# Optimization experiments

Measured on AMD Instinct MI355X. Metric: run time of the kernel, lower is better.

## Reference

```python
import jax, jax.numpy as jnp
import numpy as np

D_MODEL = 1024


def setup_inputs() -> dict:
    key = jax.random.key(0)
    ks = jax.random.split(key, 8)
    B, S, D = 2, 2048, D_MODEL
    s = 1.0 / np.sqrt(D)
    causal = jnp.where(jnp.tril(jnp.ones((S, S), dtype=bool)), 0.0, -1e9)[None, None]
    return {
        "query": jax.random.normal(ks[0], (B, S, D), jnp.float32),
        "key": jax.random.normal(ks[1], (B, S, D), jnp.float32),
        "value": jax.random.normal(ks[2], (B, S, D), jnp.float32),
        "padding_mask": jnp.zeros((B, 1, 1, S), jnp.float32),
        "lookahead_mask": causal.astype(jnp.float32),
        "w_q": jax.random.normal(ks[3], (D, D), jnp.float32) * s,
        "w_k": jax.random.normal(ks[4], (D, D), jnp.float32) * s,
        "w_v": jax.random.normal(ks[5], (D, D), jnp.float32) * s,
        "w_out": jax.random.normal(ks[6], (D, D), jnp.float32) * s,
        "b_q": jnp.zeros((D,), jnp.float32),
        "b_k": jnp.zeros((D,), jnp.float32),
        "b_v": jnp.zeros((D,), jnp.float32),
        "b_out": jnp.zeros((D,), jnp.float32),
        "n_heads": 16,
    }


def reference(query, key, value, padding_mask, lookahead_mask,
              w_q, w_k, w_v, w_out, b_q, b_k, b_v, b_out, n_heads):
    B, S, D = query.shape
    d_k = D // n_heads
    # projections (torch Linear: x @ W.T + b; here weights stored as (in, out))
    q = (query @ w_q + b_q).reshape(B, S, n_heads, d_k).transpose(0, 2, 1, 3)
    k = (key @ w_k + b_k).reshape(B, S, n_heads, d_k).transpose(0, 2, 1, 3)
    v = (value @ w_v + b_v).reshape(B, S, n_heads, d_k).transpose(0, 2, 1, 3)
    scores = jnp.einsum("bhqd,bhkd->bhqk", q, k) / jnp.sqrt(jnp.float32(d_k))
    scores = scores + padding_mask + lookahead_mask
    attn = jax.nn.softmax(scores, axis=-1)
    out = jnp.einsum("bhqk,bhkd->bhqd", attn, v)
    out = out.transpose(0, 2, 1, 3).reshape(B, S, D)
    return out @ w_out + b_out
```

## Files before the change

### kernel.cpp

```cpp
#include <hip/hip_runtime.h>
#include <hip/hip_bf16.h>
#include <stdint.h>

typedef __bf16 bf16x8 __attribute__((ext_vector_type(8)));
typedef __bf16 bf16x4 __attribute__((ext_vector_type(4)));
typedef float f32x4 __attribute__((ext_vector_type(4)));

#define DMODEL 1024
#define SEQ    2048
#define NHEAD  16
#define DK     64
#define MTOT   4096
#define KDIM   1024

#define DRAIN_VM_LGKM() asm volatile("s_waitcnt vmcnt(0) lgkmcnt(0)" ::: "memory")
#define DRAIN_LGKM()    asm volatile("s_waitcnt lgkmcnt(0)" ::: "memory")

__device__ __forceinline__ void gl2lds16(const void* g, void* l) {
  __builtin_amdgcn_global_load_lds((__attribute__((address_space(1))) void*)(g),
                                   (__attribute__((address_space(3))) void*)(l),
                                   16, 0, 0);
}

__global__ __launch_bounds__(256) void k_cvt3(const float* __restrict__ q,
                                              const float* __restrict__ k,
                                              const float* __restrict__ v,
                                              __bf16* __restrict__ oq,
                                              __bf16* __restrict__ ok,
                                              __bf16* __restrict__ ov,
                                              int n4) {
  const int which = blockIdx.y;
  const float* in = which == 0 ? q : (which == 1 ? k : v);
  __bf16* out = which == 0 ? oq : (which == 1 ? ok : ov);
  const int i = blockIdx.x * 256 + threadIdx.x;
  if (i >= n4) return;
  const float4 f = ((const float4*)in)[i];
  bf16x4 o = { (__bf16)f.x, (__bf16)f.y, (__bf16)f.z, (__bf16)f.w };
  ((bf16x4*)out)[i] = o;
}

__global__ __launch_bounds__(256) void k_transpose4(const float* __restrict__ w0,
                                                    const float* __restrict__ w1,
                                                    const float* __restrict__ w2,
                                                    const float* __restrict__ w3,
                                                    __bf16* __restrict__ t0,
                                                    __bf16* __restrict__ t1,
                                                    __bf16* __restrict__ t2,
                                                    __bf16* __restrict__ t3) {
  const int z = blockIdx.z;
  const float* W = z == 0 ? w0 : (z == 1 ? w1 : (z == 2 ? w2 : w3));
  __bf16* WT = z == 0 ? t0 : (z == 1 ? t1 : (z == 2 ? t2 : t3));
  __shared__ float tile[32][33];
  int n0 = blockIdx.x * 32, k0 = blockIdx.y * 32;
  int tx = threadIdx.x & 31, ty = threadIdx.x >> 5;
  #pragma unroll
  for (int i = ty; i < 32; i += 8)
    tile[i][tx] = W[(size_t)(k0 + i) * DMODEL + n0 + tx];
  __syncthreads();
  #pragma unroll
  for (int i = ty; i < 32; i += 8)
    WT[(size_t)(n0 + i) * DMODEL + k0 + tx] = (__bf16)tile[tx][i];
}

__global__ __launch_bounds__(256) void k_gemm_qkv(
    const __bf16* __restrict__ A0, const __bf16* __restrict__ A1, const __bf16* __restrict__ A2,
    const __bf16* __restrict__ W0, const __bf16* __restrict__ W1, const __bf16* __restrict__ W2,
    const float* __restrict__ bi0, const float* __restrict__ bi1, const float* __restrict__ bi2,
    __bf16* __restrict__ C0, __bf16* __restrict__ C1, __bf16* __restrict__ C2) {
  const int z = blockIdx.z;
  const __bf16* A  = z == 0 ? A0 : (z == 1 ? A1 : A2);
  const __bf16* BT = z == 0 ? W0 : (z == 1 ? W1 : W2);
  const float* bias = z == 0 ? bi0 : (z == 1 ? bi1 : bi2);
  __bf16* Cout = z == 0 ? C0 : (z == 1 ? C1 : C2);

  __shared__ __align__(16) __bf16 As[128 * 32];
  __shared__ __align__(16) __bf16 Bs[128 * 32];
  const int tid = threadIdx.x;
  const int lane = tid & 63;
  const int wv = tid >> 6;
  const int wm = wv >> 1, wn = wv & 1;
  const int m0 = blockIdx.y * 128, n0 = blockIdx.x * 128;
  const int lr = lane & 15, lg = lane >> 4;

  f32x4 acc[4][4] = {};

  for (int k0 = 0; k0 < KDIM; k0 += 32) {
    #pragma unroll
    for (int i = 0; i < 2; ++i) {
      int c = tid + i * 256;
      int row = c >> 2, seg = c & 3;
      gl2lds16(A + (size_t)(m0 + row) * KDIM + k0 + seg * 8, (char*)As + c * 16);
      gl2lds16(BT + (size_t)(n0 + row) * KDIM + k0 + seg * 8, (char*)Bs + c * 16);
    }
    DRAIN_VM_LGKM();
    __syncthreads();
    bf16x8 af[4], bfr[4];
    #pragma unroll
    for (int mi = 0; mi < 4; ++mi)
      af[mi] = *(const bf16x8*)&As[(wm * 64 + mi * 16 + lr) * 32 + lg * 8];
    #pragma unroll
    for (int ni = 0; ni < 4; ++ni)
      bfr[ni] = *(const bf16x8*)&Bs[(wn * 64 + ni * 16 + lr) * 32 + lg * 8];
    #pragma unroll
    for (int mi = 0; mi < 4; ++mi)
      #pragma unroll
      for (int ni = 0; ni < 4; ++ni)
        acc[mi][ni] = __builtin_amdgcn_mfma_f32_16x16x32_bf16(af[mi], bfr[ni], acc[mi][ni], 0, 0, 0);
    DRAIN_LGKM();
    __syncthreads();
  }

  #pragma unroll
  for (int mi = 0; mi < 4; ++mi)
    #pragma unroll
    for (int ni = 0; ni < 4; ++ni) {
      const int col = n0 + wn * 64 + ni * 16 + lr;
      const float bv = bias[col];
      #pragma unroll
      for (int r = 0; r < 4; ++r) {
        const int row = m0 + wm * 64 + mi * 16 + lg * 4 + r;
        float v = acc[mi][ni][r] + bv;
        const int b = row >> 11, s = row & (SEQ - 1);
        const int h = col >> 6, dd = col & (DK - 1);
        if (z == 2)
          Cout[((size_t)(b * NHEAD + h) * DK + dd) * SEQ + s] = (__bf16)v;
        else
          Cout[((size_t)(b * NHEAD + h) * SEQ + s) * DK + dd] = (__bf16)v;
      }
    }
}

__global__ __launch_bounds__(256) void k_gemm_out(const __bf16* __restrict__ A,
                                                  const __bf16* __restrict__ BT,
                                                  const float* __restrict__ bias,
                                                  float* __restrict__ Cout) {
  __shared__ __align__(16) __bf16 As[128 * 32];
  __shared__ __align__(16) __bf16 Bs[128 * 32];
  const int tid = threadIdx.x;
  const int lane = tid & 63;
  const int wv = tid >> 6;
  const int wm = wv >> 1, wn = wv & 1;
  const int m0 = blockIdx.y * 128, n0 = blockIdx.x * 128;
  const int lr = lane & 15, lg = lane >> 4;

  f32x4 acc[4][4] = {};

  for (int k0 = 0; k0 < KDIM; k0 += 32) {
    #pragma unroll
    for (int i = 0; i < 2; ++i) {
      int c = tid + i * 256;
      int row = c >> 2, seg = c & 3;
      gl2lds16(A + (size_t)(m0 + row) * KDIM + k0 + seg * 8, (char*)As + c * 16);
      gl2lds16(BT + (size_t)(n0 + row) * KDIM + k0 + seg * 8, (char*)Bs + c * 16);
    }
    DRAIN_VM_LGKM();
    __syncthreads();
    bf16x8 af[4], bfr[4];
    #pragma unroll
    for (int mi = 0; mi < 4; ++mi)
      af[mi] = *(const bf16x8*)&As[(wm * 64 + mi * 16 + lr) * 32 + lg * 8];
    #pragma unroll
    for (int ni = 0; ni < 4; ++ni)
      bfr[ni] = *(const bf16x8*)&Bs[(wn * 64 + ni * 16 + lr) * 32 + lg * 8];
    #pragma unroll
    for (int mi = 0; mi < 4; ++mi)
      #pragma unroll
      for (int ni = 0; ni < 4; ++ni)
        acc[mi][ni] = __builtin_amdgcn_mfma_f32_16x16x32_bf16(af[mi], bfr[ni], acc[mi][ni], 0, 0, 0);
    DRAIN_LGKM();
    __syncthreads();
  }

  #pragma unroll
  for (int mi = 0; mi < 4; ++mi)
    #pragma unroll
    for (int ni = 0; ni < 4; ++ni) {
      const int col = n0 + wn * 64 + ni * 16 + lr;
      const float bv = bias[col];
      #pragma unroll
      for (int r = 0; r < 4; ++r) {
        const int row = m0 + wm * 64 + mi * 16 + lg * 4 + r;
        Cout[(size_t)row * DMODEL + col] = acc[mi][ni][r] + bv;
      }
    }
}

__global__ __launch_bounds__(256, 4) void k_attn(const __bf16* __restrict__ Q,
                                                 const __bf16* __restrict__ Kt,
                                                 const __bf16* __restrict__ Vt,
                                                 const float* __restrict__ pmask,
                                                 float* __restrict__ Op0,
                                                 float* __restrict__ Op1,
                                                 float* __restrict__ ML) {
  __shared__ __align__(16) __bf16 Ks[2][64 * 64];
  __shared__ __align__(16) __bf16 Vs[2][64 * 64];
  __shared__ __align__(16) __bf16 plds[4][16 * 64];

  const int tid = threadIdx.x;
  const int lane = tid & 63, wv = tid >> 6;
  const int lr = lane & 15, lg = lane >> 4;

  const int bid = blockIdx.x;
  const int xcd = bid & 7;
  const int rdec = bid >> 3;
  const int slot = rdec >> 5;
  const int rem = rdec & 31;
  const int pair = rem >> 1;
  const int s = rem & 1;
  const int bh = slot * 8 + xcd;
  const int b = bh >> 4, h = bh & 15;

  const __bf16* Qb = Q + (size_t)bh * SEQ * DK;
  const __bf16* Kb = Kt + (size_t)bh * SEQ * DK;
  const __bf16* Vb = Vt + (size_t)bh * DK * SEQ;
  const float* pm = pmask + (size_t)b * SEQ;
  float* Op = s ? Op1 : Op0;
  const float SCL = 0.125f * 1.44269504f;
  const float L2E = 1.44269504f;

  auto stage = [&](int buf, int t) {
    #pragma unroll
    for (int i = 0; i < 2; ++i) {
      const int c = tid + i * 256;
      const int row = c >> 3;
      const int sx = ((c & 7) * 16) ^ ((row & 7) << 4);
      gl2lds16((const char*)Kb + (size_t)(t * 64 + row) * 128 + sx,
               (char*)&Ks[buf][0] + c * 16);
      gl2lds16((const char*)Vb + (size_t)row * (SEQ * 2) + (size_t)t * 128 + sx,
               (char*)&Vs[buf][0] + c * 16);
    }
  };

  for (int half = 0; half < 2; ++half) {
    const int qb = half ? (31 - pair) : pair;
    const int nt = qb + 1;
    const int QR = qb * 64 + wv * 16;

    const bf16x8 qf0 = *(const bf16x8*)&Qb[(size_t)(QR + lr) * DK + lg * 8];
    const bf16x8 qf1 = *(const bf16x8*)&Qb[(size_t)(QR + lr) * DK + 32 + lg * 8];

    float mrow = -1e30f, lrw = 0.f;
    f32x4 oacc[4] = {};

    int t = s;
    if (t < nt) {
      stage(0, t);
      DRAIN_VM_LGKM();
      __syncthreads();
    }
    int cur = 0;
    for (; t < nt; t += 2) {
      if (t + 2 < nt) stage(cur ^ 1, t + 2);
      f32x4 sc[4];
      #pragma unroll
      for (int g = 0; g < 4; ++g) {
        const int krow = g * 16 + lr;
        const int ksw = (lr & 7) << 4;
        bf16x8 kf0 = *(const bf16x8*)((const char*)&Ks[cur][0] + krow * 128 + ((lg * 16) ^ ksw));
        bf16x8 kf1 = *(const bf16x8*)((const char*)&Ks[cur][0] + krow * 128 + ((64 + lg * 16) ^ ksw));
        f32x4 a = {};
        a = __builtin_amdgcn_mfma_f32_16x16x32_bf16(kf0, qf0, a, 0, 0, 0);
        a = __builtin_amdgcn_mfma_f32_16x16x32_bf16(kf1, qf1, a, 0, 0, 0);
        sc[g] = a;
      }
      const bool edge = (t == qb);
      #pragma unroll
      for (int g = 0; g < 4; ++g) {
        const float4 pmv = *(const float4*)&pm[t * 64 + g * 16 + lg * 4];
        const float pmf[4] = {pmv.x, pmv.y, pmv.z, pmv.w};
        #pragma unroll
        for (int r = 0; r < 4; ++r) {
          float sv = sc[g][r] * SCL + pmf[r] * L2E;
          if (edge && (t * 64 + g * 16 + lg * 4 + r > QR + lr)) sv = -1e30f;
          sc[g][r] = sv;
        }
      }
      float pmax = sc[0][0];
      #pragma unroll
      for (int g = 0; g < 4; ++g)
        #pragma unroll
        for (int r = 0; r < 4; ++r) pmax = fmaxf(pmax, sc[g][r]);
      pmax = fmaxf(pmax, __shfl_xor(pmax, 16, 64));
      pmax = fmaxf(pmax, __shfl_xor(pmax, 32, 64));
      if (!__all(pmax <= mrow + 8.f)) {
        const float mnew = fmaxf(mrow, pmax);
        const float alpha = exp2f(mrow - mnew);
        mrow = mnew;
        lrw *= alpha;
        #pragma unroll
        for (int r = 0; r < 4; ++r) {
          const float av = __shfl(alpha, lg * 4 + r, 64);
          #pragma unroll
          for (int og = 0; og < 4; ++og) oacc[og][r] *= av;
        }
      }
      float psum = 0.f;
      #pragma unroll
      for (int g = 0; g < 4; ++g)
        #pragma unroll
        for (int r = 0; r < 4; ++r) {
          float p = exp2f(sc[g][r] - mrow);
          sc[g][r] = p;
          psum += p;
        }
      psum += __shfl_xor(psum, 16, 64);
      psum += __shfl_xor(psum, 32, 64);
      lrw += psum;
      #pragma unroll
      for (int g = 0; g < 4; ++g) {
        bf16x4 pk = { (__bf16)sc[g][0], (__bf16)sc[g][1], (__bf16)sc[g][2], (__bf16)sc[g][3] };
        const int byteoff = lr * 128 + ((g * 32 + lg * 8) ^ ((lr & 7) << 4));
        *(bf16x4*)((char*)plds[wv] + byteoff) = pk;
      }
      #pragma unroll
      for (int kk = 0; kk < 2; ++kk) {
        const int pboff = lr * 128 + ((kk * 64 + lg * 16) ^ ((lr & 7) << 4));
        const bf16x8 pa = *(const bf16x8*)((char*)plds[wv] + pboff);
        #pragma unroll
        for (int og = 0; og < 4; ++og) {
          const int vrow = og * 16 + lr;
          const int vsw = (vrow & 7) << 4;
          const bf16x8 vf = *(const bf16x8*)((const char*)&Vs[cur][0] + vrow * 128 + ((kk * 64 + lg * 16) ^ vsw));
          oacc[og] = __builtin_amdgcn_mfma_f32_16x16x32_bf16(pa, vf, oacc[og], 0, 0, 0);
        }
      }
      DRAIN_VM_LGKM();
      __syncthreads();
      cur ^= 1;
    }

    #pragma unroll
    for (int r = 0; r < 4; ++r) {
      const int row = QR + lg * 4 + r;
      #pragma unroll
      for (int og = 0; og < 4; ++og)
        Op[((size_t)b * SEQ + row) * DMODEL + h * DK + og * 16 + lr] = oacc[og][r];
    }
    if (lg == 0) {
      const int ri = bh * SEQ + QR + lr;
      ML[s * 131072 + ri] = mrow;
      ML[s * 131072 + 65536 + ri] = lrw;
    }
  }
}

__global__ __launch_bounds__(256) void k_merge(const float* __restrict__ Op0,
                                               const float* __restrict__ Op1,
                                               const float* __restrict__ ML,
                                               __bf16* __restrict__ Oh) {
  const int idx = blockIdx.x * 256 + threadIdx.x;
  const int row = idx >> 8;
  const int col = (idx & 255) * 4;
  const int b = row >> 11, sr = row & (SEQ - 1);
  const int h = col >> 6;
  const int ri = (b * NHEAD + h) * SEQ + sr;
  const float m0 = ML[ri], l0 = ML[65536 + ri];
  const float m1 = ML[131072 + ri], l1 = ML[196608 + ri];
  const float M = fmaxf(m0, m1);
  const float w0 = exp2f(m0 - M), w1 = exp2f(m1 - M);
  const float inv = 1.f / (l0 * w0 + l1 * w1);
  const float s0 = w0 * inv, s1 = w1 * inv;
  const size_t off = (size_t)row * DMODEL + col;
  const float4 o0 = *(const float4*)&Op0[off];
  const float4 o1 = *(const float4*)&Op1[off];
  bf16x4 o = { (__bf16)(o0.x * s0 + o1.x * s1), (__bf16)(o0.y * s0 + o1.y * s1),
               (__bf16)(o0.z * s0 + o1.z * s1), (__bf16)(o0.w * s0 + o1.w * s1) };
  *(bf16x4*)&Oh[off] = o;
}

extern "C" void kernel_launch(void* const* d_in, const int* in_sizes, int n_in,
                              void* d_out, int out_size, void* d_ws, size_t ws_size,
                              hipStream_t stream) {
  (void)in_sizes; (void)n_in; (void)out_size; (void)ws_size;
  const float* query = (const float*)d_in[0];
  const float* key   = (const float*)d_in[1];
  const float* value = (const float*)d_in[2];
  const float* pmask = (const float*)d_in[3];
  const float* w_q = (const float*)d_in[5];
  const float* w_k = (const float*)d_in[6];
  const float* w_v = (const float*)d_in[7];
  const float* w_o = (const float*)d_in[8];
  const float* b_q = (const float*)d_in[9];
  const float* b_k = (const float*)d_in[10];
  const float* b_v = (const float*)d_in[11];
  const float* b_o = (const float*)d_in[12];

  __bf16* ws = (__bf16*)d_ws;
  const size_t WSZ = (size_t)DMODEL * DMODEL;
  const size_t XSZ = (size_t)MTOT * DMODEL;
  __bf16* WTq = ws;
  __bf16* WTk = WTq + WSZ;
  __bf16* WTv = WTk + WSZ;
  __bf16* WTo = WTv + WSZ;
  __bf16* Xq  = WTo + WSZ;
  __bf16* Xk  = Xq + XSZ;
  __bf16* Xv  = Xk + XSZ;
  __bf16* Qh  = Xv + XSZ;
  __bf16* Kh  = Qh + XSZ;
  __bf16* Vh  = Kh + XSZ;
  float*  Op0 = (float*)Xk;
  float*  Op1 = (float*)(Vh + XSZ);
  float*  MLb = (float*)(Vh + XSZ + 2 * XSZ);
  __bf16* Oh  = Xq;

  dim3 blk(256);
  k_cvt3<<<dim3(4096, 3), blk, 0, stream>>>(query, key, value, Xq, Xk, Xv, (int)(XSZ / 4));
  k_transpose4<<<dim3(32, 32, 4), blk, 0, stream>>>(w_q, w_k, w_v, w_o, WTq, WTk, WTv, WTo);

  k_gemm_qkv<<<dim3(8, 32, 3), blk, 0, stream>>>(Xq, Xk, Xv, WTq, WTk, WTv,
                                                 b_q, b_k, b_v, Qh, Kh, Vh);

  k_attn<<<dim3(1024), blk, 0, stream>>>(Qh, Kh, Vh, pmask, Op0, Op1, MLb);
  k_merge<<<dim3(4096), blk, 0, stream>>>(Op0, Op1, MLb, Oh);

  k_gemm_out<<<dim3(8, 32), blk, 0, stream>>>(Oh, WTo, b_o, (float*)d_out);
}
```

Before: 151.9 us.

## Split attention KV three ways, read V from global, store bf16 partials

The attention kernel now splits each query block's KV range across three workgroups instead of two. The merge kernel combines three partial results. The V tile is no longer staged in LDS; each lane reads V fragments straight from global memory. Partial outputs are stored as bf16 rather than fp32, and the occupancy hint rises from 4 to 6. The conversion and weight-transpose kernels are fused into one launch. The aim is more parallelism, less LDS use and less partial-output traffic. The risks are uncoalesced or repeated global V loads and some precision loss in the bf16 partials.

New measurement: 194.3 us. 28.0% more time.

```diff
diff --git a/kernel.cpp b/kernel.cpp
--- a/kernel.cpp
+++ b/kernel.cpp
@@ -22,44 +22,46 @@
                                    16, 0, 0);
 }
 
-__global__ __launch_bounds__(256) void k_cvt3(const float* __restrict__ q,
+__global__ __launch_bounds__(256) void k_prep(const float* __restrict__ q,
                                               const float* __restrict__ k,
                                               const float* __restrict__ v,
                                               __bf16* __restrict__ oq,
                                               __bf16* __restrict__ ok,
                                               __bf16* __restrict__ ov,
-                                              int n4) {
-  const int which = blockIdx.y;
-  const float* in = which == 0 ? q : (which == 1 ? k : v);
-  __bf16* out = which == 0 ? oq : (which == 1 ? ok : ov);
-  const int i = blockIdx.x * 256 + threadIdx.x;
-  if (i >= n4) return;
-  const float4 f = ((const float4*)in)[i];
-  bf16x4 o = { (__bf16)f.x, (__bf16)f.y, (__bf16)f.z, (__bf16)f.w };
-  ((bf16x4*)out)[i] = o;
-}
-
-__global__ __launch_bounds__(256) void k_transpose4(const float* __restrict__ w0,
-                                                    const float* __restrict__ w1,
-                                                    const float* __restrict__ w2,
-                                                    const float* __restrict__ w3,
-                                                    __bf16* __restrict__ t0,
-                                                    __bf16* __restrict__ t1,
-                                                    __bf16* __restrict__ t2,
-                                                    __bf16* __restrict__ t3) {
-  const int z = blockIdx.z;
-  const float* W = z == 0 ? w0 : (z == 1 ? w1 : (z == 2 ? w2 : w3));
-  __bf16* WT = z == 0 ? t0 : (z == 1 ? t1 : (z == 2 ? t2 : t3));
+                                              const float* __restrict__ w0,
+                                              const float* __restrict__ w1,
+                                              const float* __restrict__ w2,
+                                              const float* __restrict__ w3,
+                                              __bf16* __restrict__ t0,
+                                              __bf16* __restrict__ t1,
+                                              __bf16* __restrict__ t2,
+                                              __bf16* __restrict__ t3) {
   __shared__ float tile[32][33];
-  int n0 = blockIdx.x * 32, k0 = blockIdx.y * 32;
-  int tx = threadIdx.x & 31, ty = threadIdx.x >> 5;
-  #pragma unroll
-  for (int i = ty; i < 32; i += 8)
-    tile[i][tx] = W[(size_t)(k0 + i) * DMODEL + n0 + tx];
-  __syncthreads();
-  #pragma unroll
-  for (int i = ty; i < 32; i += 8)
-    WT[(size_t)(n0 + i) * DMODEL + k0 + tx] = (__bf16)tile[tx][i];
+  const int bid = blockIdx.x;
+  if (bid < 12288) {
+    const int which = bid >> 12;
+    const int i = (bid & 4095) * 256 + threadIdx.x;
+    const float* in = which == 0 ? q : (which == 1 ? k : v);
+    __bf16* out = which == 0 ? oq : (which == 1 ? ok : ov);
+    const float4 f = ((const float4*)in)[i];
+    bf16x4 o = { (__bf16)f.x, (__bf16)f.y, (__bf16)f.z, (__bf16)f.w };
+    ((bf16x4*)out)[i] = o;
+  } else {
+    const int b2 = bid - 12288;
+    const int z = b2 >> 10;
+    const int t = b2 & 1023;
+    const float* W = z == 0 ? w0 : (z == 1 ? w1 : (z == 2 ? w2 : w3));
+    __bf16* WT = z == 0 ? t0 : (z == 1 ? t1 : (z == 2 ? t2 : t3));
+    const int n0 = (t & 31) * 32, k0 = (t >> 5) * 32;
+    const int tx = threadIdx.x & 31, ty = threadIdx.x >> 5;
+    #pragma unroll
+    for (int i = ty; i < 32; i += 8)
+      tile[i][tx] = W[(size_t)(k0 + i) * DMODEL + n0 + tx];
+    __syncthreads();
+    #pragma unroll
+    for (int i = ty; i < 32; i += 8)
+      WT[(size_t)(n0 + i) * DMODEL + k0 + tx] = (__bf16)tile[tx][i];
+  }
 }
 
 __global__ __launch_bounds__(256) void k_gemm_qkv(
@@ -185,15 +187,15 @@
     }
 }
 
-__global__ __launch_bounds__(256, 4) void k_attn(const __bf16* __restrict__ Q,
+__global__ __launch_bounds__(256, 6) void k_attn(const __bf16* __restrict__ Q,
                                                  const __bf16* __restrict__ Kt,
                                                  const __bf16* __restrict__ Vt,
                                                  const float* __restrict__ pmask,
-                                                 float* __restrict__ Op0,
-                                                 float* __restrict__ Op1,
+                                                 __bf16* __restrict__ Op0,
+                                                 __bf16* __restrict__ Op1,
+                                                 __bf16* __restrict__ Op2,
                                                  float* __restrict__ ML) {
   __shared__ __align__(16) __bf16 Ks[2][64 * 64];
-  __shared__ __align__(16) __bf16 Vs[2][64 * 64];
   __shared__ __align__(16) __bf16 plds[4][16 * 64];
 
   const int tid = threadIdx.x;
@@ -203,10 +205,10 @@
   const int bid = blockIdx.x;
   const int xcd = bid & 7;
   const int rdec = bid >> 3;
-  const int slot = rdec >> 5;
-  const int rem = rdec & 31;
-  const int pair = rem >> 1;
-  const int s = rem & 1;
+  const int slot = rdec / 48;
+  const int rem = rdec % 48;
+  const int pair = rem / 3;
+  const int s = rem % 3;
   const int bh = slot * 8 + xcd;
   const int b = bh >> 4, h = bh & 15;
 
@@ -214,7 +216,7 @@
   const __bf16* Kb = Kt + (size_t)bh * SEQ * DK;
   const __bf16* Vb = Vt + (size_t)bh * DK * SEQ;
   const float* pm = pmask + (size_t)b * SEQ;
-  float* Op = s ? Op1 : Op0;
+  __bf16* Op = s == 0 ? Op0 : (s == 1 ? Op1 : Op2);
   const float SCL = 0.125f * 1.44269504f;
   const float L2E = 1.44269504f;
 
@@ -226,8 +228,6 @@
       const int sx = ((c & 7) * 16) ^ ((row & 7) << 4);
       gl2lds16((const char*)Kb + (size_t)(t * 64 + row) * 128 + sx,
                (char*)&Ks[buf][0] + c * 16);
-      gl2lds16((const char*)Vb + (size_t)row * (SEQ * 2) + (size_t)t * 128 + sx,
-               (char*)&Vs[buf][0] + c * 16);
     }
   };
 
@@ -249,8 +249,8 @@
       __syncthreads();
     }
     int cur = 0;
-    for (; t < nt; t += 2) {
-      if (t + 2 < nt) stage(cur ^ 1, t + 2);
+    for (; t < nt; t += 3) {
+      if (t + 3 < nt) stage(cur ^ 1, t + 3);
       f32x4 sc[4];
       #pragma unroll
       for (int g = 0; g < 4; ++g) {
@@ -318,9 +318,7 @@
         const bf16x8 pa = *(const bf16x8*)((char*)plds[wv] + pboff);
         #pragma unroll
         for (int og = 0; og < 4; ++og) {
-          const int vrow = og * 16 + lr;
-          const int vsw = (vrow & 7) << 4;
-          const bf16x8 vf = *(const bf16x8*)((const char*)&Vs[cur][0] + vrow * 128 + ((kk * 64 + lg * 16) ^ vsw));
+          const bf16x8 vf = *(const bf16x8*)&Vb[(size_t)(og * 16 + lr) * SEQ + t * 64 + kk * 32 + lg * 8];
           oacc[og] = __builtin_amdgcn_mfma_f32_16x16x32_bf16(pa, vf, oacc[og], 0, 0, 0);
         }
       }
@@ -334,7 +332,7 @@
       const int row = QR + lg * 4 + r;
       #pragma unroll
       for (int og = 0; og < 4; ++og)
-        Op[((size_t)b * SEQ + row) * DMODEL + h * DK + og * 16 + lr] = oacc[og][r];
+        Op[((size_t)b * SEQ + row) * DMODEL + h * DK + og * 16 + lr] = (__bf16)oacc[og][r];
     }
     if (lg == 0) {
       const int ri = bh * SEQ + QR + lr;
@@ -344,8 +342,9 @@
   }
 }
 
-__global__ __launch_bounds__(256) void k_merge(const float* __restrict__ Op0,
-                                               const float* __restrict__ Op1,
+__global__ __launch_bounds__(256) void k_merge(const __bf16* __restrict__ Op0,
+                                               const __bf16* __restrict__ Op1,
+                                               const __bf16* __restrict__ Op2,
                                                const float* __restrict__ ML,
                                                __bf16* __restrict__ Oh) {
   const int idx = blockIdx.x * 256 + threadIdx.x;
@@ -354,17 +353,21 @@
   const int b = row >> 11, sr = row & (SEQ - 1);
   const int h = col >> 6;
   const int ri = (b * NHEAD + h) * SEQ + sr;
-  const float m0 = ML[ri], l0 = ML[65536 + ri];
-  const float m1 = ML[131072 + ri], l1 = ML[196608 + ri];
-  const float M = fmaxf(m0, m1);
-  const float w0 = exp2f(m0 - M), w1 = exp2f(m1 - M);
-  const float inv = 1.f / (l0 * w0 + l1 * w1);
-  const float s0 = w0 * inv, s1 = w1 * inv;
+  const float m0 = ML[ri],          l0 = ML[65536 + ri];
+  const float m1 = ML[131072 + ri], l1 = ML[131072 + 65536 + ri];
+  const float m2 = ML[262144 + ri], l2 = ML[262144 + 65536 + ri];
+  const float M = fmaxf(fmaxf(m0, m1), m2);
+  const float w0 = exp2f(m0 - M), w1 = exp2f(m1 - M), w2 = exp2f(m2 - M);
+  const float inv = 1.f / (l0 * w0 + l1 * w1 + l2 * w2);
+  const float s0 = w0 * inv, s1 = w1 * inv, s2 = w2 * inv;
   const size_t off = (size_t)row * DMODEL + col;
-  const float4 o0 = *(const float4*)&Op0[off];
-  const float4 o1 = *(const float4*)&Op1[off];
-  bf16x4 o = { (__bf16)(o0.x * s0 + o1.x * s1), (__bf16)(o0.y * s0 + o1.y * s1),
-               (__bf16)(o0.z * s0 + o1.z * s1), (__bf16)(o0.w * s0 + o1.w * s1) };
+  const bf16x4 o0 = *(const bf16x4*)&Op0[off];
+  const bf16x4 o1 = *(const bf16x4*)&Op1[off];
+  const bf16x4 o2 = *(const bf16x4*)&Op2[off];
+  bf16x4 o = { (__bf16)((float)o0[0] * s0 + (float)o1[0] * s1 + (float)o2[0] * s2),
+               (__bf16)((float)o0[1] * s0 + (float)o1[1] * s1 + (float)o2[1] * s2),
+               (__bf16)((float)o0[2] * s0 + (float)o1[2] * s1 + (float)o2[2] * s2),
+               (__bf16)((float)o0[3] * s0 + (float)o1[3] * s1 + (float)o2[3] * s2) };
   *(bf16x4*)&Oh[off] = o;
 }
 
@@ -398,20 +401,21 @@
   __bf16* Qh  = Xv + XSZ;
   __bf16* Kh  = Qh + XSZ;
   __bf16* Vh  = Kh + XSZ;
-  float*  Op0 = (float*)Xk;
-  float*  Op1 = (float*)(Vh + XSZ);
-  float*  MLb = (float*)(Vh + XSZ + 2 * XSZ);
+  __bf16* Op0 = Xk;
+  __bf16* Op1 = Xv;
+  __bf16* Op2 = Vh + XSZ;
+  float*  MLb = (float*)(Op2 + XSZ);
   __bf16* Oh  = Xq;
 
   dim3 blk(256);
-  k_cvt3<<<dim3(4096, 3), blk, 0, stream>>>(query, key, value, Xq, Xk, Xv, (int)(XSZ / 4));
-  k_transpose4<<<dim3(32, 32, 4), blk, 0, stream>>>(w_q, w_k, w_v, w_o, WTq, WTk, WTv, WTo);
+  k_prep<<<dim3(16384), blk, 0, stream>>>(query, key, value, Xq, Xk, Xv,
+                                          w_q, w_k, w_v, w_o, WTq, WTk, WTv, WTo);
 
   k_gemm_qkv<<<dim3(8, 32, 3), blk, 0, stream>>>(Xq, Xk, Xv, WTq, WTk, WTv,
                                                  b_q, b_k, b_v, Qh, Kh, Vh);
 
-  k_attn<<<dim3(1024), blk, 0, stream>>>(Qh, Kh, Vh, pmask, Op0, Op1, MLb);
-  k_merge<<<dim3(4096), blk, 0, stream>>>(Op0, Op1, MLb, Oh);
+  k_attn<<<dim3(1536), blk, 0, stream>>>(Qh, Kh, Vh, pmask, Op0, Op1, Op2, MLb);
+  k_merge<<<dim3(4096), blk, 0, stream>>>(Op0, Op1, Op2, MLb, Oh);
 
   k_gemm_out<<<dim3(8, 32), blk, 0, stream>>>(Oh, WTo, b_o, (float*)d_out);
 }
```
